# Optimization experiments

Hardware: AMD Instinct MI355X
Metric: run time of the kernel (lower is better)

The kernel has to match this reference:

```python
import jax, jax.numpy as jnp
import numpy as np

B, S, HID = 2, 4096, 640
NH, NKV, HD = 4, 1, 256
SCALING = 256.0 ** -0.5
SOFTCAP = 50.0
WINDOW = 512
EPS = 1e-6
ROPE_THETA = 10000.0  # local (sliding) rope base in Gemma3


def _rope_tables(seq_len, dim, theta):
    inv_freq = 1.0 / (theta ** (np.arange(0, dim, 2, dtype=np.float32) / dim))  # [dim/2]
    t = np.arange(seq_len, dtype=np.float32)
    freqs = np.outer(t, inv_freq)                      # [S, dim/2]
    emb = np.concatenate([freqs, freqs], axis=-1)      # [S, dim]
    return np.cos(emb)[None], np.sin(emb)[None]        # [1, S, dim]


def _sliding_causal_mask(b, s, window):
    i = np.arange(s)[:, None]
    j = np.arange(s)[None, :]
    allowed = (j <= i) & (j > i - window)              # causal + sliding window
    mask = np.where(allowed, 0.0, -1e9).astype(np.float32)
    return np.broadcast_to(mask[None, None], (b, 1, s, s)).copy()


def setup_inputs() -> dict:
    key = jax.random.key(0)
    ks = jax.random.split(key, 8)
    cos_np, sin_np = _rope_tables(S, HD, ROPE_THETA)
    return {
        "hidden_states": jax.random.normal(ks[0], (B, S, HID), jnp.float32),
        "cos": jnp.asarray(cos_np),
        "sin": jnp.asarray(sin_np),
        "attention_mask": jnp.asarray(_sliding_causal_mask(B, S, WINDOW)),
        "Wq": jax.random.normal(ks[1], (HID, NH * HD), jnp.float32) * 0.02,
        "Wk": jax.random.normal(ks[2], (HID, NKV * HD), jnp.float32) * 0.02,
        "Wv": jax.random.normal(ks[3], (HID, NKV * HD), jnp.float32) * 0.02,
        "Wo": jax.random.normal(ks[4], (NH * HD, HID), jnp.float32) * 0.02,
        "q_norm_w": jax.random.normal(ks[5], (HD,), jnp.float32) * 0.02,
        "k_norm_w": jax.random.normal(ks[6], (HD,), jnp.float32) * 0.02,
    }


def _rms_norm(x, w):
    var = jnp.mean(jnp.square(x), axis=-1, keepdims=True)
    return x * jax.lax.rsqrt(var + EPS) * (1.0 + w)


def _rotate_half(x):
    x1, x2 = jnp.split(x, 2, axis=-1)
    return jnp.concatenate([-x2, x1], axis=-1)


def _apply_rope(x, cos, sin):
    # x: [B, H, S, D]; cos/sin: [1, S, D] -> unsqueeze head dim
    c = cos[:, None, :, :]
    s = sin[:, None, :, :]
    return x * c + _rotate_half(x) * s


def reference(hidden_states, cos, sin, attention_mask, Wq, Wk, Wv, Wo, q_norm_w, k_norm_w):
    b, s, _ = hidden_states.shape
    # projections (no bias)
    q = (hidden_states @ Wq).reshape(b, s, NH, HD).transpose(0, 2, 1, 3)   # [B,NH,S,D]
    k = (hidden_states @ Wk).reshape(b, s, NKV, HD).transpose(0, 2, 1, 3)  # [B,1,S,D]
    v = (hidden_states @ Wv).reshape(b, s, NKV, HD).transpose(0, 2, 1, 3)  # [B,1,S,D]
    # per-head RMSNorm on q/k
    q = _rms_norm(q, q_norm_w)
    k = _rms_norm(k, k_norm_w)
    # RoPE
    q = _apply_rope(q, cos, sin)
    k = _apply_rope(k, cos, sin)
    # GQA: single kv head broadcast to all query heads
    k2 = k[:, 0]  # [B,S,D]
    v2 = v[:, 0]  # [B,S,D]
    scores = jnp.einsum('bhqd,bkd->bhqk', q, k2) * SCALING
    scores = SOFTCAP * jnp.tanh(scores / SOFTCAP)          # logit softcapping
    scores = scores + attention_mask                        # causal + sliding window
    attn = jax.nn.softmax(scores, axis=-1)
    out = jnp.einsum('bhqk,bkd->bhqd', attn, v2)            # [B,NH,S,D]
    out = out.transpose(0, 2, 1, 3).reshape(b, s, NH * HD)  # [B,S,NH*D]
    return out @ Wo                                         # [B,S,HID]
```

## Files before the change

kernel.cpp:

```cpp
#include <hip/hip_runtime.h>

typedef unsigned short u16;
typedef unsigned int u32;

typedef __attribute__((ext_vector_type(8)))  short bf16x8;
typedef __attribute__((ext_vector_type(4)))  float f32x4;

__device__ __forceinline__ float b2f(u16 u) {
    union { unsigned int i; float f; } v; v.i = ((unsigned int)u) << 16; return v.f;
}
__device__ __forceinline__ u16 f2b(float f) {
    union { float ff; unsigned int i; } v; v.ff = f;
    unsigned int x = v.i;
    return (u16)((x + 0x7fffu + ((x >> 16) & 1u)) >> 16);
}
__device__ __forceinline__ bool detect_bf16(const void* cosT) {
    return ((*(const u32*)cosT) & 0xffffu) == 0x3f80u;
}
__device__ __forceinline__ float4 ld4(const void* p, size_t off, bool isbf) {
    if (isbf) {
        ushort4 v = *(const ushort4*)((const u16*)p + off);
        return make_float4(b2f(v.x), b2f(v.y), b2f(v.z), b2f(v.w));
    }
    return *(const float4*)((const float*)p + off);
}
__device__ __forceinline__ float lds1(const void* p, size_t off, bool isbf) {
    return isbf ? b2f(((const u16*)p)[off]) : ((const float*)p)[off];
}
__device__ __forceinline__ void gll16(const void* g, void* l) {
    __builtin_amdgcn_global_load_lds(
        (const __attribute__((address_space(1))) u32*)g,
        (__attribute__((address_space(3))) u32*)l, 16, 0, 0);
}
__device__ __forceinline__ float capmask(float sdot, int i, int j) {
    float v = sdot * (0.0625f / 50.0f);
    v = fminf(fmaxf(v, -10.0f), 10.0f);
    float e = __expf(2.0f * v);
    float c = 50.0f * (e - 1.0f) / (e + 1.0f);
    bool allowed = (j <= i) && (j > i - 512);
    return allowed ? c : -1e30f;
}

__global__ __launch_bounds__(256) void prep(
    const void* __restrict__ hidden,
    const void* __restrict__ Wq, const void* __restrict__ Wk,
    const void* __restrict__ Wv, const void* __restrict__ Wo,
    const void* __restrict__ cosT,
    u16* __restrict__ Hb, u16* __restrict__ WT, u16* __restrict__ WoT)
{
    const bool isbf = detect_bf16(cosT);
    __shared__ float T[32][33];
    int id = blockIdx.x;
    if (id < 2560) {
        if (isbf) return;
        size_t base = ((size_t)id * 256 + threadIdx.x) * 8;
        float4 a = ld4(hidden, base, false);
        float4 b = ld4(hidden, base + 4, false);
        uint4 o;
        o.x = (u32)f2b(a.x) | ((u32)f2b(a.y) << 16);
        o.y = (u32)f2b(a.z) | ((u32)f2b(a.w) << 16);
        o.z = (u32)f2b(b.x) | ((u32)f2b(b.y) << 16);
        o.w = (u32)f2b(b.z) | ((u32)f2b(b.w) << 16);
        *(uint4*)(Hb + base) = o;
        return;
    }
    id -= 2560;
    const int tx = threadIdx.x & 31, ty = threadIdx.x >> 5;
    if (id < 960) {
        const int n0 = (id % 48) * 32, k0 = (id / 48) * 32;
        const void* src; int ldw, nof;
        if (n0 < 1024)      { src = Wq; ldw = 1024; nof = n0; }
        else if (n0 < 1280) { src = Wk; ldw = 256;  nof = n0 - 1024; }
        else                { src = Wv; ldw = 256;  nof = n0 - 1280; }
#pragma unroll
        for (int j = 0; j < 4; j++)
            T[ty + 8 * j][tx] = lds1(src, (size_t)(k0 + ty + 8 * j) * ldw + nof + tx, isbf);
        __syncthreads();
#pragma unroll
        for (int j = 0; j < 4; j++)
            WT[(size_t)(n0 + ty + 8 * j) * 640 + k0 + tx] = f2b(T[tx][ty + 8 * j]);
    } else {
        id -= 960;
        const int k0 = (id & 31) * 32, n0 = (id >> 5) * 32;
#pragma unroll
        for (int j = 0; j < 4; j++)
            T[ty + 8 * j][tx] = lds1(Wo, (size_t)(k0 + ty + 8 * j) * 640 + n0 + tx, isbf);
        __syncthreads();
#pragma unroll
        for (int j = 0; j < 4; j++)
            WoT[(size_t)(n0 + ty + 8 * j) * 1024 + k0 + tx] = f2b(T[tx][ty + 8 * j]);
    }
}

__global__ __launch_bounds__(256) void qkv_gemm(
    const void* __restrict__ hidden, const void* __restrict__ cosT,
    const u16* __restrict__ Hb, const u16* __restrict__ WT,
    u16* __restrict__ Qb, u16* __restrict__ Kb, u16* __restrict__ Vtg)
{
    const u16* Asrc = detect_bf16(cosT) ? (const u16*)hidden : Hb;
    const int n0 = blockIdx.x * 128, m0 = blockIdx.y * 128;
    const int t = threadIdx.x, w = t >> 6, lane = t & 63;
    const int l15 = lane & 15, quad = lane >> 4;
    const int wm = (w & 1) * 64, wn = (w >> 1) * 64;

    __shared__ __align__(16) char smem[33792];

    f32x4 acc[4][4];
#pragma unroll
    for (int i = 0; i < 4; i++)
#pragma unroll
        for (int j = 0; j < 4; j++) acc[i][j] = (f32x4)0.0f;

#pragma unroll
    for (int i = 0; i < 2; i++) {
        int ci = t + 256 * i, m = ci >> 2, c = ci & 3;
        gll16(Asrc + (size_t)(m0 + m) * 640 + c * 8, smem + ci * 16);
        gll16(WT + (size_t)(n0 + m) * 640 + c * 8, smem + 8192 + ci * 16);
    }
    __syncthreads();

    for (int it = 0; it < 20; ++it) {
        const int kb = it * 32;
        char* cur = smem + (it & 1) * 16384;
        if (it < 19) {
            char* nxt = smem + ((it + 1) & 1) * 16384;
#pragma unroll
            for (int i = 0; i < 2; i++) {
                int ci = t + 256 * i, m = ci >> 2, c = ci & 3;
                gll16(Asrc + (size_t)(m0 + m) * 640 + kb + 32 + c * 8, nxt + ci * 16);
                gll16(WT + (size_t)(n0 + m) * 640 + kb + 32 + c * 8, nxt + 8192 + ci * 16);
            }
        }
        const u16 (*Ah)[32] = (const u16 (*)[32])cur;
        const u16 (*Bh)[32] = (const u16 (*)[32])(cur + 8192);
        bf16x8 af[4], bfr[4];
#pragma unroll
        for (int mi = 0; mi < 4; mi++)
            af[mi] = *(const bf16x8*)&Ah[wm + mi * 16 + l15][quad * 8];
#pragma unroll
        for (int ni = 0; ni < 4; ni++)
            bfr[ni] = *(const bf16x8*)&Bh[wn + ni * 16 + l15][quad * 8];
#pragma unroll
        for (int mi = 0; mi < 4; mi++)
#pragma unroll
            for (int ni = 0; ni < 4; ni++)
                acc[mi][ni] = __builtin_amdgcn_mfma_f32_16x16x32_bf16(
                    af[mi], bfr[ni], acc[mi][ni], 0, 0, 0);
        __syncthreads();
    }

    if (n0 >= 1280) {
        const int bb = m0 >> 12, sblk = m0 & 4095;
#pragma unroll
        for (int mi = 0; mi < 4; mi++)
#pragma unroll
            for (int ni = 0; ni < 4; ni++) {
                int vd = n0 + wn + ni * 16 + l15 - 1280;
                int sb = sblk + wm + mi * 16 + quad * 4;
                ushort4 vv = make_ushort4(f2b(acc[mi][ni][0]), f2b(acc[mi][ni][1]),
                                          f2b(acc[mi][ni][2]), f2b(acc[mi][ni][3]));
                *(ushort4*)(Vtg + (size_t)bb * 1048576 + (size_t)vd * 4096 + sb) = vv;
            }
        return;
    }

    u16 (*Sc)[132] = (u16 (*)[132])smem;
#pragma unroll
    for (int mi = 0; mi < 4; mi++)
#pragma unroll
        for (int ni = 0; ni < 4; ni++)
#pragma unroll
            for (int r = 0; r < 4; r++)
                Sc[wm + mi * 16 + quad * 4 + r][wn + ni * 16 + l15] = f2b(acc[mi][ni][r]);
    __syncthreads();

    u16* dst; int ldo, coff;
    if (n0 < 1024) { dst = Qb; ldo = 1024; coff = n0; }
    else           { dst = Kb; ldo = 256;  coff = n0 - 1024; }
#pragma unroll
    for (int i = 0; i < 8; i++) {
        int idx = t + 256 * i, r = idx >> 4, c = idx & 15;
        *(uint4*)(dst + (size_t)(m0 + r) * ldo + coff + c * 8) = *(const uint4*)&Sc[r][c * 8];
    }
}

__global__ __launch_bounds__(320) void norm_rope(
    u16* __restrict__ Qb, u16* __restrict__ Kb,
    const void* __restrict__ cosT, const void* __restrict__ sinT,
    const void* __restrict__ qw, const void* __restrict__ kw)
{
    const bool isbf = detect_bf16(cosT);
    const int row = blockIdx.x, s = row & 4095;
    const int g = threadIdx.x >> 6, lane = threadIdx.x & 63, d0 = lane * 4;

    u16* p; const void* w;
    if (g < 4) { p = Qb + (size_t)row * 1024 + g * 256 + d0; w = qw; }
    else       { p = Kb + (size_t)row * 256 + d0;            w = kw; }

    ushort4 xv = *(const ushort4*)p;
    float x0 = b2f(xv.x), x1 = b2f(xv.y), x2 = b2f(xv.z), x3 = b2f(xv.w);
    float ssum = x0 * x0 + x1 * x1 + x2 * x2 + x3 * x3;
#pragma unroll
    for (int off = 32; off > 0; off >>= 1) ssum += __shfl_xor(ssum, off, 64);
    float rs = rsqrtf(ssum * (1.0f / 256.0f) + 1e-6f);

    float4 wv = ld4(w, d0, isbf);
    float n0 = x0 * rs * (1.0f + wv.x);
    float n1 = x1 * rs * (1.0f + wv.y);
    float n2 = x2 * rs * (1.0f + wv.z);
    float n3 = x3 * rs * (1.0f + wv.w);

    float o0 = __shfl_xor(n0, 32, 64);
    float o1 = __shfl_xor(n1, 32, 64);
    float o2 = __shfl_xor(n2, 32, 64);
    float o3 = __shfl_xor(n3, 32, 64);
    float sgn = (lane < 32) ? -1.0f : 1.0f;

    float4 cv = ld4(cosT, (size_t)s * 256 + d0, isbf);
    float4 sv = ld4(sinT, (size_t)s * 256 + d0, isbf);
    *(ushort4*)p = make_ushort4(
        f2b(n0 * cv.x + sgn * o0 * sv.x), f2b(n1 * cv.y + sgn * o1 * sv.y),
        f2b(n2 * cv.z + sgn * o2 * sv.z), f2b(n3 * cv.w + sgn * o3 * sv.w));
}

__global__ __launch_bounds__(512, 2) void attn_mfma(
    const u16* __restrict__ Qb, const u16* __restrict__ Kb,
    const u16* __restrict__ Vtg, u16* __restrict__ AO)
{
    const int bx = blockIdx.x;
    const int q0 = (((bx & 7) << 4) + (bx >> 3)) * 32;
    const int b  = blockIdx.y;
    const int t = threadIdx.x, w = t >> 6, lane = t & 63;
    const int h = w & 3, qh = w >> 2;
    const int l15 = lane & 15, quad = lane >> 4;
    const int qbase = q0 + qh * 16;
    const int swz = (l15 & 7) << 4;

    __shared__ __align__(16) u16 KsD[2][64][256];
    __shared__ __align__(16) u16 VtD[2][256][64];
    __shared__ __align__(16) u16 Pr[8][16][72];
    __shared__ float l_s[8][16];

    bf16x8 qf[8];
    {
        const u16* qp = Qb + ((size_t)(b * 4096 + qbase + l15)) * 1024 + h * 256 + quad * 8;
#pragma unroll
        for (int s = 0; s < 8; s++) qf[s] = *(const bf16x8*)(qp + s * 32);
    }

    f32x4 o[16];
#pragma unroll
    for (int i = 0; i < 16; i++) o[i] = (f32x4)0.0f;
    float lp[4] = {0.f, 0.f, 0.f, 0.f};

    const int lo = q0 - 511;
    const int jb0 = lo > 0 ? (lo >> 6) << 6 : 0;
    const int jb1 = (q0 + 31) & ~63;
    const int nt  = ((jb1 - jb0) >> 6) + 1;

    const u16* kbase = Kb + (size_t)b * 4096 * 256;
    const u16* vbase = Vtg + (size_t)b * 1048576;

#define STAGE_KV(jb_, bi_)                                                          \
    {                                                                               \
        char* kd = (char*)&KsD[bi_][0][0];                                          \
        char* vd = (char*)&VtD[bi_][0][0];                                          \
        _Pragma("unroll")                                                           \
        for (int i_ = 0; i_ < 4; i_++) {                                            \
            int ci = t + 512 * i_;                                                  \
            int kr = ci >> 5, kc = ci & 31;                                         \
            gll16(kbase + (size_t)((jb_) + kr) * 256 + ((kc ^ (kr & 7)) * 8),       \
                  kd + ci * 16);                                                    \
            int vr = ci >> 3, vc = ci & 7;                                          \
            gll16(vbase + (size_t)vr * 4096 + (jb_) + ((vc ^ (vr & 7)) * 8),        \
                  vd + ci * 16);                                                    \
        }                                                                           \
    }

    STAGE_KV(jb0, 0);

    for (int it = 0; it < nt; ++it) {
        const int jb = jb0 + it * 64;
        if (it + 1 < nt) {
            STAGE_KV(jb + 64, (it + 1) & 1);
            asm volatile("s_waitcnt vmcnt(8)" ::: "memory");
        } else {
            asm volatile("s_waitcnt vmcnt(0)" ::: "memory");
        }
        __builtin_amdgcn_s_barrier();
        __builtin_amdgcn_sched_barrier(0);

        const char* ksb = (const char*)&KsD[it & 1][0][0];
        const char* vtb = (const char*)&VtD[it & 1][0][0];

        f32x4 s[4];
#pragma unroll
        for (int a = 0; a < 4; a++) s[a] = (f32x4)0.0f;
#pragma unroll
        for (int ds = 0; ds < 8; ds++) {
#pragma unroll
            for (int a = 0; a < 4; a++) {
                bf16x8 kf = *(const bf16x8*)(ksb + (a * 16 + l15) * 512 +
                                             (((ds * 4 + quad) * 16) ^ swz));
                s[a] = __builtin_amdgcn_mfma_f32_16x16x32_bf16(qf[ds], kf, s[a], 0, 0, 0);
            }
        }
#pragma unroll
        for (int ap = 0; ap < 2; ap++) {
            const int j0 = jb + ap * 32 + l15;
#pragma unroll
            for (int r = 0; r < 4; r++) {
                int qi = qbase + quad * 4 + r;
                float p0 = __expf(capmask(s[2 * ap][r],     qi, j0));
                float p1 = __expf(capmask(s[2 * ap + 1][r], qi, j0 + 16));
                u16 pb0 = f2b(p0), pb1 = f2b(p1);
                Pr[w][quad * 4 + r][ap * 32 + l15]      = pb0;
                Pr[w][quad * 4 + r][ap * 32 + 16 + l15] = pb1;
                lp[r] += b2f(pb0) + b2f(pb1);
            }
        }
        __threadfence_block();
        bf16x8 pf0 = *(const bf16x8*)&Pr[w][l15][quad * 8];
        bf16x8 pf1 = *(const bf16x8*)&Pr[w][l15][32 + quad * 8];
#pragma unroll
        for (int mt = 0; mt < 16; mt++) {
            bf16x8 vf0 = *(const bf16x8*)(vtb + (mt * 16 + l15) * 128 +
                                          ((quad * 16) ^ swz));
            o[mt] = __builtin_amdgcn_mfma_f32_16x16x32_bf16(vf0, pf0, o[mt], 0, 0, 0);
        }
#pragma unroll
        for (int mt = 0; mt < 16; mt++) {
            bf16x8 vf1 = *(const bf16x8*)(vtb + (mt * 16 + l15) * 128 +
                                          (((4 + quad) * 16) ^ swz));
            o[mt] = __builtin_amdgcn_mfma_f32_16x16x32_bf16(vf1, pf1, o[mt], 0, 0, 0);
        }

        asm volatile("s_waitcnt lgkmcnt(0)" ::: "memory");
        __builtin_amdgcn_s_barrier();
        __builtin_amdgcn_sched_barrier(0);
    }
#undef STAGE_KV

#pragma unroll
    for (int r = 0; r < 4; r++) {
        float v = lp[r];
        v += __shfl_xor(v, 1, 64); v += __shfl_xor(v, 2, 64);
        v += __shfl_xor(v, 4, 64); v += __shfl_xor(v, 8, 64);
        lp[r] = v;
    }
    if (l15 == 0) {
#pragma unroll
        for (int r = 0; r < 4; r++) l_s[w][quad * 4 + r] = lp[r];
    }
    __threadfence_block();
    __syncthreads();
    const float inv = 1.0f / l_s[w][l15];

    u16* aop = AO + ((size_t)(b * 4096 + qbase + l15)) * 1024 + h * 256 + quad * 4;
#pragma unroll
    for (int mt = 0; mt < 16; mt++) {
        *(ushort4*)(aop + mt * 16) = make_ushort4(
            f2b(o[mt][0] * inv), f2b(o[mt][1] * inv),
            f2b(o[mt][2] * inv), f2b(o[mt][3] * inv));
    }
}

__global__ __launch_bounds__(256) void out_gemm(
    const u16* __restrict__ AO, const u16* __restrict__ WoT,
    const void* __restrict__ cosT, void* __restrict__ outp)
{
    const bool isbf = detect_bf16(cosT);
    const int n0 = blockIdx.x * 64, m0 = blockIdx.y * 128;
    const int t = threadIdx.x, w = t >> 6, lane = t & 63;
    const int l15 = lane & 15, quad = lane >> 4;
    const int wm = (w & 1) * 64, wn = (w >> 1) * 32;

    __shared__ __align__(16) char smem[34816];

    f32x4 acc[4][2];
#pragma unroll
    for (int i = 0; i < 4; i++)
#pragma unroll
        for (int j = 0; j < 2; j++) acc[i][j] = (f32x4)0.0f;

    {
#pragma unroll
        for (int i = 0; i < 2; i++) {
            int ci = t + 256 * i, m = ci >> 2, c = ci & 3;
            gll16(AO + (size_t)(m0 + m) * 1024 + c * 8, smem + ci * 16);
        }
        int m = t >> 2, c = t & 3;
        gll16(WoT + (size_t)(n0 + m) * 1024 + c * 8, smem + 8192 + t * 16);
    }
    __syncthreads();

    for (int it = 0; it < 32; ++it) {
        const int kb = it * 32;
        char* cur = smem + (it & 1) * 12288;
        if (it < 31) {
            char* nxt = smem + ((it + 1) & 1) * 12288;
#pragma unroll
            for (int i = 0; i < 2; i++) {
                int ci = t + 256 * i, m = ci >> 2, c = ci & 3;
                gll16(AO + (size_t)(m0 + m) * 1024 + kb + 32 + c * 8, nxt + ci * 16);
            }
            int m = t >> 2, c = t & 3;
            gll16(WoT + (size_t)(n0 + m) * 1024 + kb + 32 + c * 8, nxt + 8192 + t * 16);
        }
        const u16 (*Ah)[32] = (const u16 (*)[32])cur;
        const u16 (*Bh)[32] = (const u16 (*)[32])(cur + 8192);
        bf16x8 af[4], bfr[2];
#pragma unroll
        for (int mi = 0; mi < 4; mi++)
            af[mi] = *(const bf16x8*)&Ah[wm + mi * 16 + l15][quad * 8];
#pragma unroll
        for (int ni = 0; ni < 2; ni++)
            bfr[ni] = *(const bf16x8*)&Bh[wn + ni * 16 + l15][quad * 8];
#pragma unroll
        for (int mi = 0; mi < 4; mi++)
#pragma unroll
            for (int ni = 0; ni < 2; ni++)
                acc[mi][ni] = __builtin_amdgcn_mfma_f32_16x16x32_bf16(
                    af[mi], bfr[ni], acc[mi][ni], 0, 0, 0);
        __syncthreads();
    }

    float (*Scf)[68] = (float (*)[68])smem;
#pragma unroll
    for (int mi = 0; mi < 4; mi++)
#pragma unroll
        for (int ni = 0; ni < 2; ni++)
#pragma unroll
            for (int r = 0; r < 4; r++)
                Scf[wm + mi * 16 + quad * 4 + r][wn + ni * 16 + l15] = acc[mi][ni][r];
    __syncthreads();

    if (isbf) {
#pragma unroll
        for (int i = 0; i < 4; i++) {
            int idx = t + 256 * i, r = idx >> 3, c = idx & 7;
            ushort4 lo4 = make_ushort4(
                f2b(Scf[r][c * 8 + 0]), f2b(Scf[r][c * 8 + 1]),
                f2b(Scf[r][c * 8 + 2]), f2b(Scf[r][c * 8 + 3]));
            ushort4 hi4 = make_ushort4(
                f2b(Scf[r][c * 8 + 4]), f2b(Scf[r][c * 8 + 5]),
                f2b(Scf[r][c * 8 + 6]), f2b(Scf[r][c * 8 + 7]));
            u16* p = (u16*)outp + (size_t)(m0 + r) * 640 + n0 + c * 8;
            *(ushort4*)p = lo4; *(ushort4*)(p + 4) = hi4;
        }
    } else {
#pragma unroll
        for (int i = 0; i < 8; i++) {
            int idx = t + 256 * i, r = idx >> 4, c = idx & 15;
            float4 v = *(const float4*)&Scf[r][c * 4];
            *(float4*)((float*)outp + (size_t)(m0 + r) * 640 + n0 + c * 4) = v;
        }
    }
}

extern "C" void kernel_launch(void* const* d_in, const int* in_sizes, int n_in,
                              void* d_out, int out_size, void* d_ws, size_t ws_size,
                              hipStream_t stream) {
    const void* hidden = d_in[0];
    const void* cosT   = d_in[1];
    const void* sinT   = d_in[2];
    const void* Wq     = d_in[4];
    const void* Wk     = d_in[5];
    const void* Wv     = d_in[6];
    const void* Wo     = d_in[7];
    const void* qw     = d_in[8];
    const void* kw     = d_in[9];

    char* ws = (char*)d_ws;
    u16* Hb  = (u16*)ws;
    u16* WT  = (u16*)(ws + 10485760);
    u16* AO  = (u16*)ws;
    u16* WoT = (u16*)(ws + 16777216);
    u16* Qb  = (u16*)(ws + 18087936);
    u16* Kb  = (u16*)(ws + 34865152);
    u16* Vtg = (u16*)(ws + 39059456);

    prep<<<dim3(4160), 256, 0, stream>>>(hidden, Wq, Wk, Wv, Wo, cosT, Hb, WT, WoT);
    qkv_gemm<<<dim3(12, 64), 256, 0, stream>>>(hidden, cosT, Hb, WT, Qb, Kb, Vtg);
    norm_rope<<<dim3(8192), 320, 0, stream>>>(Qb, Kb, cosT, sinT, qw, kw);
    attn_mfma<<<dim3(128, 2), 512, 0, stream>>>(Qb, Kb, Vtg, AO);
    out_gemm<<<dim3(10, 64), 256, 0, stream>>>(AO, WoT, cosT, d_out);
}
```

Before: 311.1 us.

## Fuse output projection into attention kernel epilogue

Drops the separate out_gemm launch. Each attention block stages its normalized 32x1024 bf16 attention output in shared memory, reusing the K buffer with an XOR swizzle. It then multiplies that tile by Wo^T directly, each wave computing 80 output columns, and writes the final result. This removes the AO round trip through global memory and one kernel launch. In exchange, B fragments are read straight from global memory without LDS staging, output stores are scalar and uncoalesced, and the attention kernel holds more registers, which may hurt occupancy.

```diff
diff --git a/kernel.cpp b/kernel.cpp
--- a/kernel.cpp
+++ b/kernel.cpp
@@ -225,7 +225,8 @@
 
 __global__ __launch_bounds__(512, 2) void attn_mfma(
     const u16* __restrict__ Qb, const u16* __restrict__ Kb,
-    const u16* __restrict__ Vtg, u16* __restrict__ AO)
+    const u16* __restrict__ Vtg, const u16* __restrict__ WoT,
+    const void* __restrict__ cosT, void* __restrict__ outp)
 {
     const int bx = blockIdx.x;
     const int q0 = (((bx & 7) << 4) + (bx >> 3)) * 32;
@@ -356,105 +357,63 @@
     __syncthreads();
     const float inv = 1.0f / l_s[w][l15];
 
-    u16* aop = AO + ((size_t)(b * 4096 + qbase + l15)) * 1024 + h * 256 + quad * 4;
-#pragma unroll
-    for (int mt = 0; mt < 16; mt++) {
-        *(ushort4*)(aop + mt * 16) = make_ushort4(
-            f2b(o[mt][0] * inv), f2b(o[mt][1] * inv),
-            f2b(o[mt][2] * inv), f2b(o[mt][3] * inv));
-    }
-}
-
-__global__ __launch_bounds__(256) void out_gemm(
-    const u16* __restrict__ AO, const u16* __restrict__ WoT,
-    const void* __restrict__ cosT, void* __restrict__ outp)
-{
+    u16* Al = (u16*)&KsD[0][0][0];
+    {
+        const int arow = qh * 16 + l15;
+        char* arp = (char*)Al + arow * 2048;
+        const int rswz = (arow & 7) << 4;
+#pragma unroll
+        for (int mt = 0; mt < 16; mt++) {
+            int cb = (h * 256 + mt * 16 + quad * 4) * 2;
+            ushort4 vv = make_ushort4(
+                f2b(o[mt][0] * inv), f2b(o[mt][1] * inv),
+                f2b(o[mt][2] * inv), f2b(o[mt][3] * inv));
+            *(ushort4*)(arp + (cb ^ rswz)) = vv;
+        }
+    }
+    __syncthreads();
+
     const bool isbf = detect_bf16(cosT);
-    const int n0 = blockIdx.x * 64, m0 = blockIdx.y * 128;
-    const int t = threadIdx.x, w = t >> 6, lane = t & 63;
-    const int l15 = lane & 15, quad = lane >> 4;
-    const int wm = (w & 1) * 64, wn = (w >> 1) * 32;
-
-    __shared__ __align__(16) char smem[34816];
-
-    f32x4 acc[4][2];
-#pragma unroll
-    for (int i = 0; i < 4; i++)
-#pragma unroll
-        for (int j = 0; j < 2; j++) acc[i][j] = (f32x4)0.0f;
-
-    {
-#pragma unroll
-        for (int i = 0; i < 2; i++) {
-            int ci = t + 256 * i, m = ci >> 2, c = ci & 3;
-            gll16(AO + (size_t)(m0 + m) * 1024 + c * 8, smem + ci * 16);
-        }
-        int m = t >> 2, c = t & 3;
-        gll16(WoT + (size_t)(n0 + m) * 1024 + c * 8, smem + 8192 + t * 16);
-    }
-    __syncthreads();
-
-    for (int it = 0; it < 32; ++it) {
-        const int kb = it * 32;
-        char* cur = smem + (it & 1) * 12288;
-        if (it < 31) {
-            char* nxt = smem + ((it + 1) & 1) * 12288;
-#pragma unroll
-            for (int i = 0; i < 2; i++) {
-                int ci = t + 256 * i, m = ci >> 2, c = ci & 3;
-                gll16(AO + (size_t)(m0 + m) * 1024 + kb + 32 + c * 8, nxt + ci * 16);
-            }
-            int m = t >> 2, c = t & 3;
-            gll16(WoT + (size_t)(n0 + m) * 1024 + kb + 32 + c * 8, nxt + 8192 + t * 16);
-        }
-        const u16 (*Ah)[32] = (const u16 (*)[32])cur;
-        const u16 (*Bh)[32] = (const u16 (*)[32])(cur + 8192);
-        bf16x8 af[4], bfr[2];
-#pragma unroll
-        for (int mi = 0; mi < 4; mi++)
-            af[mi] = *(const bf16x8*)&Ah[wm + mi * 16 + l15][quad * 8];
-#pragma unroll
-        for (int ni = 0; ni < 2; ni++)
-            bfr[ni] = *(const bf16x8*)&Bh[wn + ni * 16 + l15][quad * 8];
-#pragma unroll
-        for (int mi = 0; mi < 4; mi++)
-#pragma unroll
-            for (int ni = 0; ni < 2; ni++)
-                acc[mi][ni] = __builtin_amdgcn_mfma_f32_16x16x32_bf16(
-                    af[mi], bfr[ni], acc[mi][ni], 0, 0, 0);
-        __syncthreads();
-    }
-
-    float (*Scf)[68] = (float (*)[68])smem;
-#pragma unroll
-    for (int mi = 0; mi < 4; mi++)
-#pragma unroll
-        for (int ni = 0; ni < 2; ni++)
-#pragma unroll
-            for (int r = 0; r < 4; r++)
-                Scf[wm + mi * 16 + quad * 4 + r][wn + ni * 16 + l15] = acc[mi][ni][r];
-    __syncthreads();
-
+    const u16* wrow = WoT + (size_t)(w * 80) * 1024;
+    f32x4 oc[2][5];
+#pragma unroll
+    for (int mi = 0; mi < 2; mi++)
+#pragma unroll
+        for (int ni = 0; ni < 5; ni++) oc[mi][ni] = (f32x4)0.0f;
+
+    for (int kk = 0; kk < 1024; kk += 32) {
+        const int kbyt = (kk * 2 + quad * 16) ^ swz;
+        bf16x8 af0 = *(const bf16x8*)((char*)Al + l15 * 2048 + kbyt);
+        bf16x8 af1 = *(const bf16x8*)((char*)Al + (16 + l15) * 2048 + kbyt);
+#pragma unroll
+        for (int ni = 0; ni < 5; ni++) {
+            bf16x8 bf2 = *(const bf16x8*)(wrow + (size_t)(ni * 16 + l15) * 1024 + kk + quad * 8);
+            oc[0][ni] = __builtin_amdgcn_mfma_f32_16x16x32_bf16(af0, bf2, oc[0][ni], 0, 0, 0);
+            oc[1][ni] = __builtin_amdgcn_mfma_f32_16x16x32_bf16(af1, bf2, oc[1][ni], 0, 0, 0);
+        }
+    }
+
+    const size_t rb = (size_t)(b * 4096 + q0);
     if (isbf) {
-#pragma unroll
-        for (int i = 0; i < 4; i++) {
-            int idx = t + 256 * i, r = idx >> 3, c = idx & 7;
-            ushort4 lo4 = make_ushort4(
-                f2b(Scf[r][c * 8 + 0]), f2b(Scf[r][c * 8 + 1]),
-                f2b(Scf[r][c * 8 + 2]), f2b(Scf[r][c * 8 + 3]));
-            ushort4 hi4 = make_ushort4(
-                f2b(Scf[r][c * 8 + 4]), f2b(Scf[r][c * 8 + 5]),
-                f2b(Scf[r][c * 8 + 6]), f2b(Scf[r][c * 8 + 7]));
-            u16* p = (u16*)outp + (size_t)(m0 + r) * 640 + n0 + c * 8;
-            *(ushort4*)p = lo4; *(ushort4*)(p + 4) = hi4;
-        }
+        u16* op = (u16*)outp;
+#pragma unroll
+        for (int mi = 0; mi < 2; mi++)
+#pragma unroll
+            for (int ni = 0; ni < 5; ni++)
+#pragma unroll
+                for (int r = 0; r < 4; r++)
+                    op[(rb + mi * 16 + quad * 4 + r) * 640 + w * 80 + ni * 16 + l15] =
+                        f2b(oc[mi][ni][r]);
     } else {
-#pragma unroll
-        for (int i = 0; i < 8; i++) {
-            int idx = t + 256 * i, r = idx >> 4, c = idx & 15;
-            float4 v = *(const float4*)&Scf[r][c * 4];
-            *(float4*)((float*)outp + (size_t)(m0 + r) * 640 + n0 + c * 4) = v;
-        }
+        float* op = (float*)outp;
+#pragma unroll
+        for (int mi = 0; mi < 2; mi++)
+#pragma unroll
+            for (int ni = 0; ni < 5; ni++)
+#pragma unroll
+                for (int r = 0; r < 4; r++)
+                    op[(rb + mi * 16 + quad * 4 + r) * 640 + w * 80 + ni * 16 + l15] =
+                        oc[mi][ni][r];
     }
 }
 
@@ -474,7 +433,6 @@
     char* ws = (char*)d_ws;
     u16* Hb  = (u16*)ws;
     u16* WT  = (u16*)(ws + 10485760);
-    u16* AO  = (u16*)ws;
     u16* WoT = (u16*)(ws + 16777216);
     u16* Qb  = (u16*)(ws + 18087936);
     u16* Kb  = (u16*)(ws + 34865152);
@@ -483,6 +441,5 @@
     prep<<<dim3(4160), 256, 0, stream>>>(hidden, Wq, Wk, Wv, Wo, cosT, Hb, WT, WoT);
     qkv_gemm<<<dim3(12, 64), 256, 0, stream>>>(hidden, cosT, Hb, WT, Qb, Kb, Vtg);
     norm_rope<<<dim3(8192), 320, 0, stream>>>(Qb, Kb, cosT, sinT, qw, kw);
-    attn_mfma<<<dim3(128, 2), 512, 0, stream>>>(Qb, Kb, Vtg, AO);
-    out_gemm<<<dim3(10, 64), 256, 0, stream>>>(AO, WoT, cosT, d_out);
-}
+    attn_mfma<<<dim3(128, 2), 512, 0, stream>>>(Qb, Kb, Vtg, WoT, cosT, d_out);
+}
```

Result: slower. 318.9 us (+2.5%).
